# Optimization experiments

Hardware: AMD Instinct MI355X
Metric: run time of the kernel (lower is better)

## Reference

```python
import jax, jax.numpy as jnp
import numpy as np

N = 50000   # nodes
E = 800000  # edges (before self-loops)
DIN = 128
H, C = 4, 32
HC = H * C  # 128
DE = 3      # edge feature dim
G = 64      # graphs in batch
HID = 32
DOUT = 1
LN_EPS = 1e-5


def setup_inputs() -> dict:
    key = jax.random.key(0)
    ks = iter(jax.random.split(key, 64))
    def nrm(shape, s=0.1):
        return jax.random.normal(next(ks), shape, dtype=jnp.float32) * s
    inp = {}
    inp["x"] = jax.random.normal(next(ks), (N, DIN), dtype=jnp.float32)
    inp["edge_index"] = jax.random.randint(next(ks), (2, E), 0, N, dtype=jnp.int32)
    inp["batch"] = jnp.sort(jax.random.randint(next(ks), (N,), 0, G, dtype=jnp.int32))
    inp["edge_attr"] = jax.random.normal(next(ks), (E, DE), dtype=jnp.float32)
    # GATv2 layers: layer0 in=DIN(128); layers 1,2 in=HC(128)
    for l, din in enumerate([DIN, HC, HC]):
        inp[f"Wl{l}"] = nrm((HC, din)); inp[f"bl{l}"] = jnp.zeros((HC,), jnp.float32)
        inp[f"Wr{l}"] = nrm((HC, din)); inp[f"br{l}"] = jnp.zeros((HC,), jnp.float32)
        inp[f"We{l}"] = nrm((HC, DE))
        inp[f"att{l}"] = nrm((H, C))
        inp[f"bo{l}"] = jnp.zeros((HC,), jnp.float32)
    for l in range(2):
        inp[f"ln{l}_g"] = jnp.ones((HC,), jnp.float32)
        inp[f"ln{l}_b"] = jnp.zeros((HC,), jnp.float32)
    # post-processing MLP: 128->32->32->32->1
    inp["pw1"] = nrm((HID, HC)); inp["pb1"] = jnp.zeros((HID,), jnp.float32)
    inp["pw2"] = nrm((HID, HID)); inp["pb2"] = jnp.zeros((HID,), jnp.float32)
    inp["pw3"] = nrm((HID, HID)); inp["pb3"] = jnp.zeros((HID,), jnp.float32)
    inp["pw4"] = nrm((DOUT, HID)); inp["pb4"] = jnp.zeros((DOUT,), jnp.float32)
    return inp


def _gat_layer(x, src, dst, eattr, Wl, bl, Wr, br, We, att, bo):
    # GATv2Conv (concat heads). x_l from lin_l -> source, x_r from lin_r -> target.
    xl = (x @ Wl.T + bl).reshape(-1, H, C)
    xr = (x @ Wr.T + br).reshape(-1, H, C)
    e = (eattr @ We.T).reshape(-1, H, C)
    m = jax.nn.leaky_relu(xl[src] + xr[dst] + e, negative_slope=0.2)  # [E',H,C]
    s = jnp.einsum('ehc,hc->eh', m, att)                              # [E',H]
    smax = jax.ops.segment_max(s, dst, num_segments=N)
    ex = jnp.exp(s - smax[dst])
    den = jax.ops.segment_sum(ex, dst, num_segments=N)
    alpha = ex / (den[dst] + 1e-16)
    out = jax.ops.segment_sum(alpha[:, :, None] * xl[src], dst, num_segments=N)
    return out.reshape(-1, HC) + bo


def _ln(x, g, b):
    mu = jnp.mean(x, axis=-1, keepdims=True)
    var = jnp.mean((x - mu) ** 2, axis=-1, keepdims=True)
    return (x - mu) * jax.lax.rsqrt(var + LN_EPS) * g + b


def _forward(x, edge_attr, edge_index, batch, p):
    src0, dst0 = edge_index[0], edge_index[1]
    # PyG add_self_loops with fill_value='mean': per-dst-node mean of edge_attr
    cnt = jax.ops.segment_sum(jnp.ones((E,), jnp.float32), dst0, num_segments=N)
    loop_attr = jax.ops.segment_sum(edge_attr, dst0, num_segments=N) / jnp.maximum(cnt, 1.0)[:, None]
    ar = jnp.arange(N, dtype=src0.dtype)
    src = jnp.concatenate([src0, ar]); dst = jnp.concatenate([dst0, ar])
    ea = jnp.concatenate([edge_attr, loop_attr], axis=0)
    embedding = x
    for l in range(3):
        x = _gat_layer(x, src, dst, ea, p[f"Wl{l}"], p[f"bl{l}"], p[f"Wr{l}"],
                       p[f"br{l}"], p[f"We{l}"], p[f"att{l}"], p[f"bo{l}"])
        embedding = x
        x = jax.nn.relu(x)  # dropout inactive (eval)
        if l != 2:
            x = _ln(x, p[f"ln{l}_g"], p[f"ln{l}_b"])
    pooled = jax.ops.segment_max(x, batch, num_segments=G)
    pooled = jnp.where(jnp.isfinite(pooled), pooled, 0.0)
    h = jax.nn.relu(pooled @ p["pw1"].T + p["pb1"])
    h = jax.nn.relu(h @ p["pw2"].T + p["pb2"])
    h = jax.nn.relu(h @ p["pw3"].T + p["pb3"])
    out = h @ p["pw4"].T + p["pb4"]
    return embedding, out


def reference(x, edge_index, batch, edge_attr,
              Wl0, bl0, Wr0, br0, We0, att0, bo0,
              Wl1, bl1, Wr1, br1, We1, att1, bo1,
              Wl2, bl2, Wr2, br2, We2, att2, bo2,
              ln0_g, ln0_b, ln1_g, ln1_b,
              pw1, pb1, pw2, pb2, pw3, pb3, pw4, pb4):
    p = dict(Wl0=Wl0, bl0=bl0, Wr0=Wr0, br0=br0, We0=We0, att0=att0, bo0=bo0,
             Wl1=Wl1, bl1=bl1, Wr1=Wr1, br1=br1, We1=We1, att1=att1, bo1=bo1,
             Wl2=Wl2, bl2=bl2, Wr2=Wr2, br2=br2, We2=We2, att2=att2, bo2=bo2,
             ln0_g=ln0_g, ln0_b=ln0_b, ln1_g=ln1_g, ln1_b=ln1_b,
             pw1=pw1, pb1=pb1, pw2=pw2, pb2=pb2, pw3=pw3, pb3=pb3, pw4=pw4, pb4=pb4)
    return _forward(x, edge_attr, edge_index, batch, p)
```

## Files before the change

### kernel.cpp

```cpp
#include <hip/hip_runtime.h>
#include <math.h>


#define LN_EPS 1e-5f
#define LOG2E 1.44269504088896340736f
#define CHUNK 4096
#define BCAP 8192

typedef short bf16x8 __attribute__((ext_vector_type(8)));
typedef float f32x4 __attribute__((ext_vector_type(4)));
typedef float f32x2 __attribute__((ext_vector_type(2)));

static __device__ __forceinline__ unsigned short f2bf(float f) {
  unsigned int u = __float_as_uint(f);
  u += 0x7fffu + ((u >> 16) & 1u);
  return (unsigned short)(u >> 16);
}

static __device__ __forceinline__ float dpp_sum8(float v) {
  int x;
  x = __builtin_amdgcn_update_dpp(0, __float_as_int(v), 0x0B1, 0xf, 0xf, true);
  v += __int_as_float(x);
  x = __builtin_amdgcn_update_dpp(0, __float_as_int(v), 0x04E, 0xf, 0xf, true);
  v += __int_as_float(x);
  x = __builtin_amdgcn_update_dpp(0, __float_as_int(v), 0x141, 0xf, 0xf, true);
  v += __int_as_float(x);
  return v;
}


__global__ __launch_bounds__(256) void k_binA(const int* __restrict__ ei, const float* __restrict__ ea,
                                              int* __restrict__ gcnt, float4* __restrict__ staged,
                                              int E, int nbuk) {
  __shared__ int hist[256];
  __shared__ int basebuf[256];
  int t = threadIdx.x;
  int e0 = blockIdx.x * CHUNK;

  hist[t] = 0;
  __syncthreads();
#pragma unroll
  for (int i = 0; i < CHUNK / 256; ++i) {
    int e = e0 + i * 256 + t;
    if (e < E) atomicAdd(&hist[ei[E + e] >> 8], 1);
  }
  __syncthreads();
  int h = hist[t];
  if (t < nbuk && h > 0) basebuf[t] = t * BCAP + atomicAdd(&gcnt[t], h);
  hist[t] = 0;
  __syncthreads();
#pragma unroll
  for (int i = 0; i < CHUNK / 256; ++i) {
    int e = e0 + i * 256 + t;
    if (e < E) {
      int s = ei[e];
      int d = ei[E + e];
      int b = d >> 8;
      int r = atomicAdd(&hist[b], 1);
      float4 rec;
      rec.x = ea[e * 3 + 0];
      rec.y = ea[e * 3 + 1];
      rec.z = ea[e * 3 + 2];
      rec.w = __int_as_float(s | (d << 16));
      staged[basebuf[b] + r] = rec;
    }
  }
}

__global__ void k_bscan(const int* __restrict__ gcnt, int* __restrict__ bukStart,
                        int* __restrict__ offs, float4* __restrict__ e4,
                        int N, int nbuk, int EP) {
  __shared__ int sh[256];
  int t = threadIdx.x;
  int nodes = (t < nbuk) ? min(256, N - t * 256) : 0;
  int v = (t < nbuk) ? gcnt[t] + nodes : 0;
  sh[t] = v;
  __syncthreads();
  for (int d = 1; d < 256; d <<= 1) {
    int add = (t >= d) ? sh[t - d] : 0;
    __syncthreads();
    sh[t] += add;
    __syncthreads();
  }
  if (t < nbuk) bukStart[t] = sh[t] - v;
  if (t == 0) offs[N] = EP;
  if (t < 8) {
    float4 r;
    r.x = 0.f; r.y = 0.f; r.z = 0.f;
    r.w = __int_as_float(0);
    e4[EP + t] = r;
  }
}

__global__ __launch_bounds__(256) void k_binB(const float4* __restrict__ staged,
                                              const int* __restrict__ gcnt,
                                              const int* __restrict__ bukStart,
                                              float4* __restrict__ e4,
                                              int* __restrict__ offs, int N) {
  __shared__ int hist[256], cur[256], begS[256], sh[256];
  int t = threadIdx.x;
  int b = blockIdx.x;
  int n0 = b * 256;
  int nn = min(256, N - n0);
  int m = gcnt[b];
  size_t sbase = (size_t)b * BCAP;

  hist[t] = 0;
  __syncthreads();
  for (int p = t; p < m; p += 256) {
    unsigned int u = (unsigned int)__float_as_int(staged[sbase + p].w);
    atomicAdd(&hist[(int)(u >> 16) - n0], 1);
  }
  __syncthreads();
  int v = (t < nn) ? hist[t] + 1 : 0;
  sh[t] = v;
  __syncthreads();
  for (int d = 1; d < 256; d <<= 1) {
    int add = (t >= d) ? sh[t - d] : 0;
    __syncthreads();
    sh[t] += add;
    __syncthreads();
  }
  if (t < nn) {
    int base = bukStart[b] + sh[t] - v;
    cur[t] = base;
    begS[t] = base;
    offs[n0 + t] = base;
  }
  __syncthreads();
  for (int p = t; p < m; p += 256) {
    float4 rec = staged[sbase + p];
    unsigned int u = (unsigned int)__float_as_int(rec.w);
    int pos = atomicAdd(&cur[(int)(u >> 16) - n0], 1);
    rec.w = __int_as_float((int)(u & 0xffffu) * 256);
    e4[pos] = rec;
  }
  __syncthreads();
  if (t < nn) {
    int beg = begS[t], last = cur[t];
    float s0 = 0.f, s1 = 0.f, s2 = 0.f;
    for (int p = beg; p < last; ++p) {
      float4 r = e4[p];
      s0 += r.x;
      s1 += r.y;
      s2 += r.z;
    }
    float invc = 1.0f / fmaxf((float)(last - beg), 1.0f);
    float4 r;
    r.x = s0 * invc;
    r.y = s1 * invc;
    r.z = s2 * invc;
    r.w = __int_as_float((n0 + t) * 256);
    e4[last] = r;
  }
}


__global__ void k_convx(const float* __restrict__ x, unsigned short* __restrict__ xb, int n) {
  int i = (blockIdx.x * blockDim.x + threadIdx.x) * 4;
  if (i >= n) return;
  float4 v = *(const float4*)&x[i];
  ushort4 o;
  o.x = f2bf(v.x); o.y = f2bf(v.y); o.z = f2bf(v.z); o.w = f2bf(v.w);
  *(ushort4*)&xb[i] = o;
}

__global__ void k_convW(const float* __restrict__ w0, const float* __restrict__ w1,
                        const float* __restrict__ w2, const float* __restrict__ w3,
                        const float* __restrict__ w4, const float* __restrict__ w5,
                        unsigned short* __restrict__ dst) {
  const float* srcs[6] = {w0, w1, w2, w3, w4, w5};
  const float* s = srcs[blockIdx.y];
  int i = blockIdx.x * 256 + threadIdx.x;
  dst[(size_t)blockIdx.y * 16384 + i] = f2bf(s[i]);
}

__global__ void k_pack(const float* __restrict__ We0, const float* __restrict__ att0,
                       const float* __restrict__ We1, const float* __restrict__ att1,
                       const float* __restrict__ We2, const float* __restrict__ att2,
                       float* __restrict__ tab) {
  int l = blockIdx.x;
  int t = threadIdx.x;
  const float* We = (l == 0) ? We0 : ((l == 1) ? We1 : We2);
  const float* att = (l == 0) ? att0 : ((l == 1) ? att1 : att2);
  float* o = tab + (size_t)l * 512 + t * 16;
#pragma unroll
  for (int j = 0; j < 4; ++j) {
    o[j] = We[(t * 4 + j) * 3 + 0];
    o[4 + j] = We[(t * 4 + j) * 3 + 1];
    o[8 + j] = We[(t * 4 + j) * 3 + 2];
    o[12 + j] = att[t * 4 + j] * LOG2E;
  }
}

__global__ __launch_bounds__(256) void k_gemm_mfma(const unsigned short* __restrict__ xb,
                                                   const unsigned short* __restrict__ Wb,
                                                   const float* __restrict__ bl, const float* __restrict__ br,
                                                   unsigned short* __restrict__ xlb,
                                                   unsigned short* __restrict__ xrb, int N) {
  int wave = threadIdx.x >> 6;
  int lane = threadIdx.x & 63;
  int which = blockIdx.y;
  const unsigned short* W = Wb + (size_t)which * 16384;
  const float* bias = which ? br : bl;
  unsigned short* out = which ? xrb : xlb;

  int row0 = (blockIdx.x * 4 + wave) * 16;
  if (row0 >= N) return;
  int m = lane & 15;
  int q = lane >> 4;

  int brow = row0 + m;
  if (brow >= N) brow = N - 1;
  const unsigned short* xrow = xb + (size_t)brow * 128 + q * 8;

  bf16x8 bfrag[4];
#pragma unroll
  for (int kt = 0; kt < 4; ++kt) bfrag[kt] = *(const bf16x8*)(xrow + kt * 32);

  f32x4 acc[8];
#pragma unroll
  for (int jt = 0; jt < 8; ++jt) acc[jt] = (f32x4){0.f, 0.f, 0.f, 0.f};

  const unsigned short* wbase = W + (size_t)m * 128 + q * 8;
#pragma unroll
  for (int kt = 0; kt < 4; ++kt) {
#pragma unroll
    for (int jt = 0; jt < 8; ++jt) {
      bf16x8 a = *(const bf16x8*)(wbase + (size_t)jt * 16 * 128 + kt * 32);
      acc[jt] = __builtin_amdgcn_mfma_f32_16x16x32_bf16(a, bfrag[kt], acc[jt], 0, 0, 0);
    }
  }

  int node = row0 + m;
  if (node < N) {
    unsigned short* orow = out + (size_t)node * 128 + q * 4;
#pragma unroll
    for (int jt = 0; jt < 8; ++jt) {
      float4 bs = *(const float4*)&bias[jt * 16 + q * 4];
      uint2 pack;
      pack.x = (unsigned int)f2bf(acc[jt][0] + bs.x) | ((unsigned int)f2bf(acc[jt][1] + bs.y) << 16);
      pack.y = (unsigned int)f2bf(acc[jt][2] + bs.z) | ((unsigned int)f2bf(acc[jt][3] + bs.w) << 16);
      *(uint2*)(orow + jt * 16) = pack;
    }
  }
}

__global__ __launch_bounds__(256) void k_agg(const unsigned short* __restrict__ xlb,
                                             const unsigned short* __restrict__ xrb,
                                             const float4* __restrict__ e4,
                                             const int* __restrict__ offs,
                                             const float* __restrict__ scoreTab,
                                             const float* __restrict__ bo,
                                             const float* __restrict__ lng, const float* __restrict__ lnb,
                                             unsigned short* __restrict__ xnext_bf,
                                             float* __restrict__ emb, int last, int N) {
  int w = (blockIdx.x * blockDim.x + threadIdx.x) >> 6;
  if (w >= N) return;
  int lane = threadIdx.x & 63;
  int half = lane >> 5;
  int sl = lane & 31;
  int c = sl * 4;
  unsigned int c2 = (unsigned int)(c * 2);
  int beg = offs[w], end = offs[w + 1];
  int cnt = end - beg;

  f32x2 xr01, xr23, wea01, wea23, web01, web23, wec01, wec23, at01, at23;
  {
    const float4* tp = (const float4*)(scoreTab + (size_t)sl * 16);
    float4 pa = tp[0], pb = tp[1], pc = tp[2], pt = tp[3];
    wea01[0] = pa.x; wea01[1] = pa.y; wea23[0] = pa.z; wea23[1] = pa.w;
    web01[0] = pb.x; web01[1] = pb.y; web23[0] = pb.z; web23[1] = pb.w;
    wec01[0] = pc.x; wec01[1] = pc.y; wec23[0] = pc.z; wec23[1] = pc.w;
    at01[0] = pt.x; at01[1] = pt.y; at23[0] = pt.z; at23[1] = pt.w;
    uint2 vr = *(const uint2*)&xrb[(size_t)w * 128 + c];
    xr01[0] = __uint_as_float(vr.x << 16);
    xr01[1] = __uint_as_float(vr.x & 0xffff0000u);
    xr23[0] = __uint_as_float(vr.y << 16);
    xr23[1] = __uint_as_float(vr.y & 0xffff0000u);
  }

  const char* e4B = (const char*)e4;
  const char* xlL = (const char*)xlb + c2;

  float l = 0.f;
  f32x2 acc01 = {0.f, 0.f}, acc23 = {0.f, 0.f};

  int T = (cnt + 1) >> 1;

  auto compute = [&](const float4& e, uint2 v, bool valid) {
    f32x2 xl01, xl23;
    xl01[0] = __uint_as_float(v.x << 16);
    xl01[1] = __uint_as_float(v.x & 0xffff0000u);
    xl23[0] = __uint_as_float(v.y << 16);
    xl23[1] = __uint_as_float(v.y & 0xffff0000u);
    f32x2 ex = {e.x, e.x}, ey = {e.y, e.y}, ez = {e.z, e.z};
    f32x2 t01 = __builtin_elementwise_fma(wea01, ex,
                  __builtin_elementwise_fma(web01, ey,
                    __builtin_elementwise_fma(wec01, ez, xr01 + xl01)));
    f32x2 t23 = __builtin_elementwise_fma(wea23, ex,
                  __builtin_elementwise_fma(web23, ey,
                    __builtin_elementwise_fma(wec23, ez, xr23 + xl23)));
    t01 = __builtin_elementwise_max(t01, t01 * 0.2f);
    t23 = __builtin_elementwise_max(t23, t23 * 0.2f);
    f32x2 d2 = __builtin_elementwise_fma(t01, at01, t23 * at23);
    float s = d2[0] + d2[1];
    float wgt = __builtin_amdgcn_exp2f(dpp_sum8(s));
    if (!valid) wgt = 0.f;
    l += wgt;
    f32x2 w2 = {wgt, wgt};
    acc01 = __builtin_elementwise_fma(xl01, w2, acc01);
    acc23 = __builtin_elementwise_fma(xl23, w2, acc23);
  };

  unsigned int o = (unsigned int)(beg + half) << 4;
  float4 e0 = *(const float4*)(e4B + o);
  float4 e1 = *(const float4*)(e4B + o + 32u);
  o += 64u;
  uint2 g0 = *(const uint2*)(xlL + (unsigned int)__float_as_int(e0.w));

  for (int it = 0; it < T - 1; ++it) {
    float4 e2 = *(const float4*)(e4B + o);
    o += 32u;
    uint2 g1 = *(const uint2*)(xlL + (unsigned int)__float_as_int(e1.w));
    __builtin_amdgcn_sched_barrier(0);
    compute(e0, g0, true);
    e0 = e1;
    e1 = e2;
    g0 = g1;
  }
  {
    int idx = 2 * (T - 1) + half;
    compute(e0, g0, idx < cnt);
  }

  l += __shfl_xor(l, 32);
  float a0 = acc01[0]; a0 += __shfl_xor(a0, 32);
  float a1 = acc01[1]; a1 += __shfl_xor(a1, 32);
  float a2 = acc23[0]; a2 += __shfl_xor(a2, 32);
  float a3 = acc23[1]; a3 += __shfl_xor(a3, 32);

  float inv = 1.0f / l;
  f32x4 o4;
  const float4 bo4 = *(const float4*)&bo[c];
  o4[0] = a0 * inv + bo4.x;
  o4[1] = a1 * inv + bo4.y;
  o4[2] = a2 * inv + bo4.z;
  o4[3] = a3 * inv + bo4.w;

  if (last) {
    if (half == 0) {
      float4 st = {o4[0], o4[1], o4[2], o4[3]};
      *(float4*)&emb[(size_t)w * 128 + c] = st;
    }
  } else {
    f32x4 r;
    r[0] = fmaxf(o4[0], 0.f);
    r[1] = fmaxf(o4[1], 0.f);
    r[2] = fmaxf(o4[2], 0.f);
    r[3] = fmaxf(o4[3], 0.f);
    float s = r[0] + r[1] + r[2] + r[3];
    s += __shfl_xor(s, 1);
    s += __shfl_xor(s, 2);
    s += __shfl_xor(s, 4);
    s += __shfl_xor(s, 8);
    s += __shfl_xor(s, 16);
    float mu = s * 0.0078125f;
    f32x4 d;
    d[0] = r[0] - mu;
    d[1] = r[1] - mu;
    d[2] = r[2] - mu;
    d[3] = r[3] - mu;
    float v2 = d[0] * d[0] + d[1] * d[1] + d[2] * d[2] + d[3] * d[3];
    v2 += __shfl_xor(v2, 1);
    v2 += __shfl_xor(v2, 2);
    v2 += __shfl_xor(v2, 4);
    v2 += __shfl_xor(v2, 8);
    v2 += __shfl_xor(v2, 16);
    float var = v2 * 0.0078125f;
    float rstd = rsqrtf(var + LN_EPS);
    if (half == 0) {
      const float4 g4 = *(const float4*)&lng[c];
      const float4 b4 = *(const float4*)&lnb[c];
      float o0 = d[0] * rstd * g4.x + b4.x;
      float o1 = d[1] * rstd * g4.y + b4.y;
      float o2 = d[2] * rstd * g4.z + b4.z;
      float o3 = d[3] * rstd * g4.w + b4.w;
      uint2 pack;
      pack.x = (unsigned int)f2bf(o0) | ((unsigned int)f2bf(o1) << 16);
      pack.y = (unsigned int)f2bf(o2) | ((unsigned int)f2bf(o3) << 16);
      *(uint2*)&xnext_bf[(size_t)w * 128 + c] = pack;
    }
  }
}

__global__ void k_pool(const float* __restrict__ emb, const int* __restrict__ batch,
                       float* __restrict__ pooled, int N) {
  int c = threadIdx.x & 127;
  int half = threadIdx.x >> 7;
  int base = blockIdx.x * 64 + half;
  int limit = min(blockIdx.x * 64 + 64, N);
  float cur = 0.f;
  int curg = -1;
  for (int n = base; n < limit; n += 2) {
    int g = batch[n];
    if (g != curg) {
      if (curg >= 0) atomicMax((unsigned int*)&pooled[curg * 128 + c], __float_as_uint(cur));
      curg = g;
      cur = 0.f;
    }
    cur = fmaxf(cur, emb[(size_t)n * 128 + c]);
  }
  if (curg >= 0) atomicMax((unsigned int*)&pooled[curg * 128 + c], __float_as_uint(cur));
}

__global__ void k_mlp(const float* __restrict__ pooled,
                      const float* __restrict__ pw1, const float* __restrict__ pb1,
                      const float* __restrict__ pw2, const float* __restrict__ pb2,
                      const float* __restrict__ pw3, const float* __restrict__ pb3,
                      const float* __restrict__ pw4, const float* __restrict__ pb4,
                      float* __restrict__ out) {
  int g = blockIdx.x;
  int t = threadIdx.x;
  __shared__ float buf1[32], buf2[32];
  if (t < 32) {
    float acc = pb1[t];
    for (int k = 0; k < 128; ++k) acc += pw1[t * 128 + k] * pooled[g * 128 + k];
    buf1[t] = fmaxf(acc, 0.f);
  }
  __syncthreads();
  if (t < 32) {
    float acc = pb2[t];
    for (int k = 0; k < 32; ++k) acc += pw2[t * 32 + k] * buf1[k];
    buf2[t] = fmaxf(acc, 0.f);
  }
  __syncthreads();
  if (t < 32) {
    float acc = pb3[t];
    for (int k = 0; k < 32; ++k) acc += pw3[t * 32 + k] * buf2[k];
    buf1[t] = fmaxf(acc, 0.f);
  }
  __syncthreads();
  if (t == 0) {
    float acc = pb4[0];
    for (int k = 0; k < 32; ++k) acc += pw4[k] * buf1[k];
    out[g] = acc;
  }
}


extern "C" void kernel_launch(void* const* d_in, const int* in_sizes, int n_in,
                              void* d_out, int out_size, void* d_ws, size_t ws_size,
                              hipStream_t stream) {
  const float* x_in = (const float*)d_in[0];
  const int* ei = (const int*)d_in[1];
  const int* batch = (const int*)d_in[2];
  const float* ea = (const float*)d_in[3];

  const int N = in_sizes[0] / 128;
  const int E = in_sizes[1] / 2;
  const int EP = E + N;
  const int G = out_size - N * 128;
  const int NBUK = (N + 255) / 256;

  const float *Wl[3], *bl[3], *Wr[3], *br[3], *We[3], *att[3], *bo[3];
  for (int l = 0; l < 3; ++l) {
    Wl[l] = (const float*)d_in[4 + 7 * l];
    bl[l] = (const float*)d_in[5 + 7 * l];
    Wr[l] = (const float*)d_in[6 + 7 * l];
    br[l] = (const float*)d_in[7 + 7 * l];
    We[l] = (const float*)d_in[8 + 7 * l];
    att[l] = (const float*)d_in[9 + 7 * l];
    bo[l] = (const float*)d_in[10 + 7 * l];
  }
  const float* lng[2] = {(const float*)d_in[25], (const float*)d_in[27]};
  const float* lnb[2] = {(const float*)d_in[26], (const float*)d_in[28]};
  const float* pw1 = (const float*)d_in[29];
  const float* pb1 = (const float*)d_in[30];
  const float* pw2 = (const float*)d_in[31];
  const float* pb2 = (const float*)d_in[32];
  const float* pw3 = (const float*)d_in[33];
  const float* pb3 = (const float*)d_in[34];
  const float* pw4 = (const float*)d_in[35];
  const float* pb4 = (const float*)d_in[36];

  char* base = (char*)d_ws;
  size_t cur = 0;
  auto carve = [&](size_t bytes) -> char* {
    char* p = base + cur;
    cur += (bytes + 255) & ~(size_t)255;
    return p;
  };
  unsigned short* xlb = (unsigned short*)carve((size_t)N * 128 * 2);
  unsigned short* xrb = (unsigned short*)carve((size_t)N * 128 * 2);
  unsigned short* xb = (unsigned short*)carve((size_t)N * 128 * 2);
  unsigned short* Wb = (unsigned short*)carve((size_t)6 * 16384 * 2);
  float4* e4 = (float4*)carve((size_t)(EP + 8) * 16);
  float4* staged = (float4*)carve((size_t)NBUK * BCAP * 16);
  int* offs = (int*)carve((size_t)(N + 1) * 4);
  int* gcnt = (int*)carve((size_t)NBUK * 4);
  int* bukStart = (int*)carve((size_t)(NBUK + 1) * 4);
  float* scoreTab = (float*)carve((size_t)3 * 512 * 4);
  float* pooled = (float*)carve((size_t)G * 128 * 4);

  float* emb_out = (float*)d_out;
  float* mlp_out = (float*)d_out + (size_t)N * 128;

  hipMemsetAsync(gcnt, 0, (size_t)NBUK * 4, stream);
  hipMemsetAsync(pooled, 0, (size_t)G * 128 * 4, stream);

  k_binA<<<(E + CHUNK - 1) / CHUNK, 256, 0, stream>>>(ei, ea, gcnt, staged, E, NBUK);
  k_bscan<<<1, 256, 0, stream>>>(gcnt, bukStart, offs, e4, N, NBUK, EP);
  k_binB<<<NBUK, 256, 0, stream>>>(staged, gcnt, bukStart, e4, offs, N);

  k_convx<<<(N * 128 / 4 + 255) / 256, 256, 0, stream>>>(x_in, xb, N * 128);
  {
    dim3 g(64, 6);
    k_convW<<<g, 256, 0, stream>>>(Wl[0], Wr[0], Wl[1], Wr[1], Wl[2], Wr[2], Wb);
  }
  k_pack<<<3, 32, 0, stream>>>(We[0], att[0], We[1], att[1], We[2], att[2], scoreTab);

  for (int l = 0; l < 3; ++l) {
    dim3 ggrid((N + 63) / 64, 2);
    k_gemm_mfma<<<ggrid, 256, 0, stream>>>(xb, Wb + (size_t)l * 32768, bl[l], br[l], xlb, xrb, N);
    int last = (l == 2) ? 1 : 0;
    const float* g = last ? bo[l] : lng[l];
    const float* b = last ? bo[l] : lnb[l];
    k_agg<<<(N * 64 + 255) / 256, 256, 0, stream>>>(xlb, xrb, e4, offs,
                                                    scoreTab + (size_t)l * 512,
                                                    bo[l], g, b,
                                                    xb, emb_out, last, N);
  }

  k_pool<<<(N + 63) / 64, 256, 0, stream>>>(emb_out, batch, pooled, N);
  k_mlp<<<G, 64, 0, stream>>>(pooled, pw1, pb1, pw2, pb2, pw3, pb3, pw4, pb4, mlp_out);
}
```

Measured before the change: 505.8 us.

## Process four edges per wave in GAT aggregation with 8 channels per lane

The aggregation kernel now splits each wave into four 16-lane groups, each handling one edge at a time with 8 channels per lane. Previously it used two 32-lane halves with 4 channels per lane. Gathers become 16-byte loads, the head reduction shrinks to two DPP steps, and the final cross-group sum uses ds_swizzle plus shfl. The score table is repacked to 8 channels per lane to match. The goal is to halve the loop trip count per node and widen memory accesses, at the cost of more registers, dropping the explicit two-deep prefetch, and more waste on nodes with low degree.

```diff
diff --git a/kernel.cpp b/kernel.cpp
--- a/kernel.cpp
+++ b/kernel.cpp
@@ -17,15 +17,28 @@
   return (unsigned short)(u >> 16);
 }
 
-static __device__ __forceinline__ float dpp_sum8(float v) {
-  int x;
-  x = __builtin_amdgcn_update_dpp(0, __float_as_int(v), 0x0B1, 0xf, 0xf, true);
-  v += __int_as_float(x);
-  x = __builtin_amdgcn_update_dpp(0, __float_as_int(v), 0x04E, 0xf, 0xf, true);
-  v += __int_as_float(x);
-  x = __builtin_amdgcn_update_dpp(0, __float_as_int(v), 0x141, 0xf, 0xf, true);
-  v += __int_as_float(x);
+template <int CTRL>
+static __device__ __forceinline__ float dpp_add(float v) {
+  int x = __builtin_amdgcn_update_dpp(0, __float_as_int(v), CTRL, 0xf, 0xf, true);
+  return v + __int_as_float(x);
+}
+
+static __device__ __forceinline__ float dpp_sum4(float v) {
+  v = dpp_add<0x0B1>(v);
+  v = dpp_add<0x04E>(v);
   return v;
+}
+
+static __device__ __forceinline__ float dpp_sum16(float v) {
+  v = dpp_add<0x0B1>(v);
+  v = dpp_add<0x04E>(v);
+  v = dpp_add<0x141>(v);
+  v = dpp_add<0x140>(v);
+  return v;
+}
+
+static __device__ __forceinline__ float swz16(float v) {
+  return __int_as_float(__builtin_amdgcn_ds_swizzle(__float_as_int(v), 0x401F));
 }
 
 
@@ -183,13 +196,14 @@
   int t = threadIdx.x;
   const float* We = (l == 0) ? We0 : ((l == 1) ? We1 : We2);
   const float* att = (l == 0) ? att0 : ((l == 1) ? att1 : att2);
-  float* o = tab + (size_t)l * 512 + t * 16;
-#pragma unroll
-  for (int j = 0; j < 4; ++j) {
-    o[j] = We[(t * 4 + j) * 3 + 0];
-    o[4 + j] = We[(t * 4 + j) * 3 + 1];
-    o[8 + j] = We[(t * 4 + j) * 3 + 2];
-    o[12 + j] = att[t * 4 + j] * LOG2E;
+  float* o = tab + (size_t)l * 512 + t * 32;
+#pragma unroll
+  for (int j = 0; j < 8; ++j) {
+    int ch = t * 8 + j;
+    o[j] = We[ch * 3 + 0];
+    o[8 + j] = We[ch * 3 + 1];
+    o[16 + j] = We[ch * 3 + 2];
+    o[24 + j] = att[ch] * LOG2E;
   }
 }
 
@@ -258,138 +272,137 @@
   int w = (blockIdx.x * blockDim.x + threadIdx.x) >> 6;
   if (w >= N) return;
   int lane = threadIdx.x & 63;
-  int half = lane >> 5;
-  int sl = lane & 31;
-  int c = sl * 4;
-  unsigned int c2 = (unsigned int)(c * 2);
+  int g = lane >> 4;
+  int sub = lane & 15;
+  unsigned int cOff = (unsigned int)(sub * 16);
   int beg = offs[w], end = offs[w + 1];
   int cnt = end - beg;
 
-  f32x2 xr01, xr23, wea01, wea23, web01, web23, wec01, wec23, at01, at23;
+  f32x2 wea[4], web[4], wec[4], at[4], xr[4];
   {
-    const float4* tp = (const float4*)(scoreTab + (size_t)sl * 16);
-    float4 pa = tp[0], pb = tp[1], pc = tp[2], pt = tp[3];
-    wea01[0] = pa.x; wea01[1] = pa.y; wea23[0] = pa.z; wea23[1] = pa.w;
-    web01[0] = pb.x; web01[1] = pb.y; web23[0] = pb.z; web23[1] = pb.w;
-    wec01[0] = pc.x; wec01[1] = pc.y; wec23[0] = pc.z; wec23[1] = pc.w;
-    at01[0] = pt.x; at01[1] = pt.y; at23[0] = pt.z; at23[1] = pt.w;
-    uint2 vr = *(const uint2*)&xrb[(size_t)w * 128 + c];
-    xr01[0] = __uint_as_float(vr.x << 16);
-    xr01[1] = __uint_as_float(vr.x & 0xffff0000u);
-    xr23[0] = __uint_as_float(vr.y << 16);
-    xr23[1] = __uint_as_float(vr.y & 0xffff0000u);
+    const float4* tp = (const float4*)(scoreTab + (size_t)sub * 32);
+    float4 a0 = tp[0], a1 = tp[1], b0 = tp[2], b1 = tp[3];
+    float4 c0 = tp[4], c1 = tp[5], t0 = tp[6], t1 = tp[7];
+    wea[0] = (f32x2){a0.x, a0.y}; wea[1] = (f32x2){a0.z, a0.w};
+    wea[2] = (f32x2){a1.x, a1.y}; wea[3] = (f32x2){a1.z, a1.w};
+    web[0] = (f32x2){b0.x, b0.y}; web[1] = (f32x2){b0.z, b0.w};
+    web[2] = (f32x2){b1.x, b1.y}; web[3] = (f32x2){b1.z, b1.w};
+    wec[0] = (f32x2){c0.x, c0.y}; wec[1] = (f32x2){c0.z, c0.w};
+    wec[2] = (f32x2){c1.x, c1.y}; wec[3] = (f32x2){c1.z, c1.w};
+    at[0] = (f32x2){t0.x, t0.y}; at[1] = (f32x2){t0.z, t0.w};
+    at[2] = (f32x2){t1.x, t1.y}; at[3] = (f32x2){t1.z, t1.w};
+    uint4 vr = *(const uint4*)((const char*)xrb + (size_t)w * 256 + cOff);
+    xr[0][0] = __uint_as_float(vr.x << 16); xr[0][1] = __uint_as_float(vr.x & 0xffff0000u);
+    xr[1][0] = __uint_as_float(vr.y << 16); xr[1][1] = __uint_as_float(vr.y & 0xffff0000u);
+    xr[2][0] = __uint_as_float(vr.z << 16); xr[2][1] = __uint_as_float(vr.z & 0xffff0000u);
+    xr[3][0] = __uint_as_float(vr.w << 16); xr[3][1] = __uint_as_float(vr.w & 0xffff0000u);
   }
 
   const char* e4B = (const char*)e4;
-  const char* xlL = (const char*)xlb + c2;
+  const char* xlB = (const char*)xlb + cOff;
 
   float l = 0.f;
-  f32x2 acc01 = {0.f, 0.f}, acc23 = {0.f, 0.f};
-
-  int T = (cnt + 1) >> 1;
-
-  auto compute = [&](const float4& e, uint2 v, bool valid) {
-    f32x2 xl01, xl23;
-    xl01[0] = __uint_as_float(v.x << 16);
-    xl01[1] = __uint_as_float(v.x & 0xffff0000u);
-    xl23[0] = __uint_as_float(v.y << 16);
-    xl23[1] = __uint_as_float(v.y & 0xffff0000u);
+  f32x2 acc[4] = {(f32x2){0.f, 0.f}, (f32x2){0.f, 0.f}, (f32x2){0.f, 0.f}, (f32x2){0.f, 0.f}};
+
+  int Tq = (cnt + 3) >> 2;
+
+  auto compute = [&](const float4& e, uint4 v, float msk) {
+    f32x2 xl[4];
+    xl[0][0] = __uint_as_float(v.x << 16); xl[0][1] = __uint_as_float(v.x & 0xffff0000u);
+    xl[1][0] = __uint_as_float(v.y << 16); xl[1][1] = __uint_as_float(v.y & 0xffff0000u);
+    xl[2][0] = __uint_as_float(v.z << 16); xl[2][1] = __uint_as_float(v.z & 0xffff0000u);
+    xl[3][0] = __uint_as_float(v.w << 16); xl[3][1] = __uint_as_float(v.w & 0xffff0000u);
     f32x2 ex = {e.x, e.x}, ey = {e.y, e.y}, ez = {e.z, e.z};
-    f32x2 t01 = __builtin_elementwise_fma(wea01, ex,
-                  __builtin_elementwise_fma(web01, ey,
-                    __builtin_elementwise_fma(wec01, ez, xr01 + xl01)));
-    f32x2 t23 = __builtin_elementwise_fma(wea23, ex,
-                  __builtin_elementwise_fma(web23, ey,
-                    __builtin_elementwise_fma(wec23, ez, xr23 + xl23)));
-    t01 = __builtin_elementwise_max(t01, t01 * 0.2f);
-    t23 = __builtin_elementwise_max(t23, t23 * 0.2f);
-    f32x2 d2 = __builtin_elementwise_fma(t01, at01, t23 * at23);
-    float s = d2[0] + d2[1];
-    float wgt = __builtin_amdgcn_exp2f(dpp_sum8(s));
-    if (!valid) wgt = 0.f;
+    f32x2 part = {0.f, 0.f};
+#pragma unroll
+    for (int j = 0; j < 4; ++j) {
+      f32x2 t = __builtin_elementwise_fma(wea[j], ex,
+                  __builtin_elementwise_fma(web[j], ey,
+                    __builtin_elementwise_fma(wec[j], ez, xr[j] + xl[j])));
+      t = __builtin_elementwise_max(t, t * 0.2f);
+      part = __builtin_elementwise_fma(t, at[j], part);
+    }
+    float s = dpp_sum4(part[0] + part[1]);
+    float wgt = __builtin_amdgcn_exp2f(s) * msk;
     l += wgt;
     f32x2 w2 = {wgt, wgt};
-    acc01 = __builtin_elementwise_fma(xl01, w2, acc01);
-    acc23 = __builtin_elementwise_fma(xl23, w2, acc23);
+#pragma unroll
+    for (int j = 0; j < 4; ++j) acc[j] = __builtin_elementwise_fma(xl[j], w2, acc[j]);
   };
 
-  unsigned int o = (unsigned int)(beg + half) << 4;
-  float4 e0 = *(const float4*)(e4B + o);
-  float4 e1 = *(const float4*)(e4B + o + 32u);
-  o += 64u;
-  uint2 g0 = *(const uint2*)(xlL + (unsigned int)__float_as_int(e0.w));
-
-  for (int it = 0; it < T - 1; ++it) {
-    float4 e2 = *(const float4*)(e4B + o);
-    o += 32u;
-    uint2 g1 = *(const uint2*)(xlL + (unsigned int)__float_as_int(e1.w));
-    __builtin_amdgcn_sched_barrier(0);
-    compute(e0, g0, true);
-    e0 = e1;
-    e1 = e2;
-    g0 = g1;
+  unsigned int o = (unsigned int)(beg + g) << 4;
+  float4 eC = *(const float4*)(e4B + o);
+#pragma unroll 2
+  for (int it = 0; it < Tq - 1; ++it) {
+    uint4 v = *(const uint4*)(xlB + (unsigned int)__float_as_int(eC.w));
+    float4 eN = *(const float4*)(e4B + o + 64u);
+    o += 64u;
+    compute(eC, v, 1.f);
+    eC = eN;
   }
   {
-    int idx = 2 * (T - 1) + half;
-    compute(e0, g0, idx < cnt);
-  }
-
-  l += __shfl_xor(l, 32);
-  float a0 = acc01[0]; a0 += __shfl_xor(a0, 32);
-  float a1 = acc01[1]; a1 += __shfl_xor(a1, 32);
-  float a2 = acc23[0]; a2 += __shfl_xor(a2, 32);
-  float a3 = acc23[1]; a3 += __shfl_xor(a3, 32);
+    uint4 v = *(const uint4*)(xlB + (unsigned int)__float_as_int(eC.w));
+    float msk = (4 * (Tq - 1) + g < cnt) ? 1.f : 0.f;
+    compute(eC, v, msk);
+  }
+
+  float a0 = acc[0][0], a1 = acc[0][1], a2 = acc[1][0], a3 = acc[1][1];
+  float a4 = acc[2][0], a5 = acc[2][1], a6 = acc[3][0], a7 = acc[3][1];
+  l += swz16(l); l += __shfl_xor(l, 32);
+  a0 += swz16(a0); a0 += __shfl_xor(a0, 32);
+  a1 += swz16(a1); a1 += __shfl_xor(a1, 32);
+  a2 += swz16(a2); a2 += __shfl_xor(a2, 32);
+  a3 += swz16(a3); a3 += __shfl_xor(a3, 32);
+  a4 += swz16(a4); a4 += __shfl_xor(a4, 32);
+  a5 += swz16(a5); a5 += __shfl_xor(a5, 32);
+  a6 += swz16(a6); a6 += __shfl_xor(a6, 32);
+  a7 += swz16(a7); a7 += __shfl_xor(a7, 32);
 
   float inv = 1.0f / l;
-  f32x4 o4;
-  const float4 bo4 = *(const float4*)&bo[c];
-  o4[0] = a0 * inv + bo4.x;
-  o4[1] = a1 * inv + bo4.y;
-  o4[2] = a2 * inv + bo4.z;
-  o4[3] = a3 * inv + bo4.w;
+  const float4 bo0 = *(const float4*)&bo[sub * 8];
+  const float4 bo1 = *(const float4*)&bo[sub * 8 + 4];
+  float o0 = a0 * inv + bo0.x, o1 = a1 * inv + bo0.y;
+  float o2 = a2 * inv + bo0.z, o3 = a3 * inv + bo0.w;
+  float o4 = a4 * inv + bo1.x, o5 = a5 * inv + bo1.y;
+  float o6 = a6 * inv + bo1.z, o7 = a7 * inv + bo1.w;
 
   if (last) {
-    if (half == 0) {
-      float4 st = {o4[0], o4[1], o4[2], o4[3]};
-      *(float4*)&emb[(size_t)w * 128 + c] = st;
+    if (g == 0) {
+      float* er = &emb[(size_t)w * 128 + sub * 8];
+      *(float4*)er = (float4){o0, o1, o2, o3};
+      *(float4*)(er + 4) = (float4){o4, o5, o6, o7};
     }
   } else {
-    f32x4 r;
-    r[0] = fmaxf(o4[0], 0.f);
-    r[1] = fmaxf(o4[1], 0.f);
-    r[2] = fmaxf(o4[2], 0.f);
-    r[3] = fmaxf(o4[3], 0.f);
-    float s = r[0] + r[1] + r[2] + r[3];
-    s += __shfl_xor(s, 1);
-    s += __shfl_xor(s, 2);
-    s += __shfl_xor(s, 4);
-    s += __shfl_xor(s, 8);
-    s += __shfl_xor(s, 16);
+    float r0 = fmaxf(o0, 0.f), r1 = fmaxf(o1, 0.f), r2 = fmaxf(o2, 0.f), r3 = fmaxf(o3, 0.f);
+    float r4 = fmaxf(o4, 0.f), r5 = fmaxf(o5, 0.f), r6 = fmaxf(o6, 0.f), r7 = fmaxf(o7, 0.f);
+    float s = ((r0 + r1) + (r2 + r3)) + ((r4 + r5) + (r6 + r7));
+    s = dpp_sum16(s);
     float mu = s * 0.0078125f;
-    f32x4 d;
-    d[0] = r[0] - mu;
-    d[1] = r[1] - mu;
-    d[2] = r[2] - mu;
-    d[3] = r[3] - mu;
-    float v2 = d[0] * d[0] + d[1] * d[1] + d[2] * d[2] + d[3] * d[3];
-    v2 += __shfl_xor(v2, 1);
-    v2 += __shfl_xor(v2, 2);
-    v2 += __shfl_xor(v2, 4);
-    v2 += __shfl_xor(v2, 8);
-    v2 += __shfl_xor(v2, 16);
-    float var = v2 * 0.0078125f;
-    float rstd = rsqrtf(var + LN_EPS);
-    if (half == 0) {
-      const float4 g4 = *(const float4*)&lng[c];
-      const float4 b4 = *(const float4*)&lnb[c];
-      float o0 = d[0] * rstd * g4.x + b4.x;
-      float o1 = d[1] * rstd * g4.y + b4.y;
-      float o2 = d[2] * rstd * g4.z + b4.z;
-      float o3 = d[3] * rstd * g4.w + b4.w;
-      uint2 pack;
-      pack.x = (unsigned int)f2bf(o0) | ((unsigned int)f2bf(o1) << 16);
-      pack.y = (unsigned int)f2bf(o2) | ((unsigned int)f2bf(o3) << 16);
-      *(uint2*)&xnext_bf[(size_t)w * 128 + c] = pack;
+    float d0 = r0 - mu, d1 = r1 - mu, d2 = r2 - mu, d3 = r3 - mu;
+    float d4 = r4 - mu, d5 = r5 - mu, d6 = r6 - mu, d7 = r7 - mu;
+    float v2 = ((d0 * d0 + d1 * d1) + (d2 * d2 + d3 * d3)) +
+               ((d4 * d4 + d5 * d5) + (d6 * d6 + d7 * d7));
+    v2 = dpp_sum16(v2);
+    float rstd = rsqrtf(v2 * 0.0078125f + LN_EPS);
+    if (g == 0) {
+      const float4 g0v = *(const float4*)&lng[sub * 8];
+      const float4 g1v = *(const float4*)&lng[sub * 8 + 4];
+      const float4 b0v = *(const float4*)&lnb[sub * 8];
+      const float4 b1v = *(const float4*)&lnb[sub * 8 + 4];
+      float y0 = d0 * rstd * g0v.x + b0v.x;
+      float y1 = d1 * rstd * g0v.y + b0v.y;
+      float y2 = d2 * rstd * g0v.z + b0v.z;
+      float y3 = d3 * rstd * g0v.w + b0v.w;
+      float y4 = d4 * rstd * g1v.x + b1v.x;
+      float y5 = d5 * rstd * g1v.y + b1v.y;
+      float y6 = d6 * rstd * g1v.z + b1v.z;
+      float y7 = d7 * rstd * g1v.w + b1v.w;
+      uint4 pack;
+      pack.x = (unsigned int)f2bf(y0) | ((unsigned int)f2bf(y1) << 16);
+      pack.y = (unsigned int)f2bf(y2) | ((unsigned int)f2bf(y3) << 16);
+      pack.z = (unsigned int)f2bf(y4) | ((unsigned int)f2bf(y5) << 16);
+      pack.w = (unsigned int)f2bf(y6) | ((unsigned int)f2bf(y7) << 16);
+      *(uint4*)&xnext_bf[(size_t)w * 128 + sub * 8] = pack;
     }
   }
 }
@@ -518,7 +531,7 @@
     dim3 g(64, 6);
     k_convW<<<g, 256, 0, stream>>>(Wl[0], Wr[0], Wl[1], Wr[1], Wl[2], Wr[2], Wb);
   }
-  k_pack<<<3, 32, 0, stream>>>(We[0], att[0], We[1], att[1], We[2], att[2], scoreTab);
+  k_pack<<<3, 16, 0, stream>>>(We[0], att[0], We[1], att[1], We[2], att[2], scoreTab);
 
   for (int l = 0; l < 3; ++l) {
     dim3 ggrid((N + 63) / 64, 2);
```

Result: slower. 608.5 us (+20.3%).
